# Kernel tuning notes

Hardware: AMD Instinct MI355X
Metric: run time of the kernel (lower is better)

The kernel has to match this reference:

```python
import jax, jax.numpy as jnp
import numpy as np

E = 8           # num_local_experts
H = 1024        # hidden_size
F = 1024        # moe_ffn_hidden_size (per-half; fc1 out = 2*F due to GLU)
T = 16384       # total dispatched tokens
GLU_LINEAR_OFFSET = 1.0


def setup_inputs() -> dict:
    key = jax.random.key(0)
    ks = jax.random.split(key, 7)
    s1 = 1.0 / np.sqrt(H)
    s2 = 1.0 / np.sqrt(F)
    return {
        "hidden_states": jax.random.normal(ks[0], (T, H), jnp.float32),
        "tokens_per_expert": jnp.full((E,), T // E, dtype=jnp.int64),
        "probs": jax.random.uniform(ks[1], (T,), jnp.float32),
        # expert params; torch Linear W is [out,in], stored here as [in,out] (same math)
        "W1": jax.random.uniform(ks[2], (E, H, 2 * F), jnp.float32, -s1, s1),
        "b1": jax.random.uniform(ks[3], (E, 2 * F), jnp.float32, -s1, s1),
        "W2": jax.random.uniform(ks[4], (E, F, H), jnp.float32, -s2, s2),
        "b2": jax.random.uniform(ks[5], (E, H), jnp.float32, -s2, s2),
    }


def reference(hidden_states, tokens_per_expert, probs, W1, b1, W2, b2):
    # Tokens arrive grouped contiguously by expert with equal counts (as in
    # setup_inputs), so the split/loop/cat in the torch module is exactly a
    # reshape + grouped (batched) GEMM over the expert axis.
    e = W1.shape[0]
    t, h = hidden_states.shape
    x = hidden_states.reshape(e, t // e, h)            # [E, Tpe, H]
    p = probs.reshape(e, t // e)                       # [E, Tpe]
    # fc1 (gated)
    y = jnp.einsum('eth,ehf->etf', x, W1) + b1[:, None, :]  # [E, Tpe, 2F]
    gate, lin = jnp.split(y, 2, axis=-1)
    a = jax.nn.silu(gate) * (lin + GLU_LINEAR_OFFSET)       # [E, Tpe, F]
    a = a * p[..., None]                                    # per-token scale
    # fc2
    out = jnp.einsum('etf,efh->eth', a, W2) + b2[:, None, :]
    return out.reshape(t, h)
```

## Files before the change

kernel.cpp:

```cpp
#include <hip/hip_runtime.h>
#include <hip/hip_bf16.h>
#include <stdint.h>

#define T_TOK 16384
#define H_DIM 1024
#define F_DIM 1024
#define E_NUM 8
#define TPE   2048


typedef unsigned short u16;
typedef __attribute__((ext_vector_type(8))) short bf16x8;
typedef __attribute__((ext_vector_type(4))) float f32x4;
typedef __attribute__((ext_vector_type(8))) u16 u16x8;

__device__ __forceinline__ u16 f2bf(float x) {
  unsigned int u = __float_as_uint(x);
  u = (u + 0x7fffu + ((u >> 16) & 1u)) >> 16;
  return (u16)u;
}

#define GLD16(gp, lp)                                                          \
  __builtin_amdgcn_global_load_lds(                                            \
      (const __attribute__((address_space(1))) void*)(gp),                     \
      (__attribute__((address_space(3))) void*)(lp), 16, 0, 0)

#define VMW(N) asm volatile("s_waitcnt vmcnt(" #N ")" ::: "memory");

__global__ __launch_bounds__(256) void prep_all(
    const float* __restrict__ x, const float* __restrict__ W1,
    const float* __restrict__ W2, u16* __restrict__ xbf,
    u16* __restrict__ w1t, u16* __restrict__ w2t) {
  __shared__ float tile[64][65];
  const int bid = blockIdx.x;
  const int t = threadIdx.x;

  if (bid < 4096) {
    size_t base = (size_t)bid * 4096 + (size_t)t * 16;
    const float4* s = (const float4*)(x + base);
    float4 v0 = s[0], v1 = s[1], v2 = s[2], v3 = s[3];
    u16x8 o0, o1;
    o0[0] = f2bf(v0.x); o0[1] = f2bf(v0.y); o0[2] = f2bf(v0.z); o0[3] = f2bf(v0.w);
    o0[4] = f2bf(v1.x); o0[5] = f2bf(v1.y); o0[6] = f2bf(v1.z); o0[7] = f2bf(v1.w);
    o1[0] = f2bf(v2.x); o1[1] = f2bf(v2.y); o1[2] = f2bf(v2.z); o1[3] = f2bf(v2.w);
    o1[4] = f2bf(v3.x); o1[5] = f2bf(v3.y); o1[6] = f2bf(v3.z); o1[7] = f2bf(v3.w);
    *(u16x8*)(xbf + base) = o0;
    *(u16x8*)(xbf + base + 8) = o1;
    return;
  }

  const float* src; u16* dst; int R, C, e, rt, ct;
  if (bid < 8192) {
    int id = bid - 4096;
    e = id >> 9; int r2 = id & 511; rt = r2 >> 5; ct = r2 & 31;
    src = W1; dst = w1t; R = H_DIM; C = 2 * F_DIM;
  } else {
    int id = bid - 8192;
    e = id >> 8; int r2 = id & 255; rt = r2 >> 4; ct = r2 & 15;
    src = W2; dst = w2t; R = F_DIM; C = H_DIM;
  }
  const float* s = src + (size_t)e * R * C + (size_t)(rt << 6) * C + (ct << 6);
  int lr = t >> 4, lc = (t & 15) << 2;
#pragma unroll
  for (int i = 0; i < 4; i++) {
    float4 v = *(const float4*)(s + (size_t)(lr + i * 16) * C + lc);
    tile[lr + i * 16][lc + 0] = v.x;
    tile[lr + i * 16][lc + 1] = v.y;
    tile[lr + i * 16][lc + 2] = v.z;
    tile[lr + i * 16][lc + 3] = v.w;
  }
  __syncthreads();
  u16* d = dst + (size_t)e * C * R + (size_t)(ct << 6) * R + (rt << 6);
  int orow = t >> 2, ok = (t & 3) << 4;
  u16x8 o0, o1;
#pragma unroll
  for (int i = 0; i < 8; i++) o0[i] = f2bf(tile[ok + i][orow]);
#pragma unroll
  for (int i = 0; i < 8; i++) o1[i] = f2bf(tile[ok + 8 + i][orow]);
  *(u16x8*)(d + (size_t)orow * R + ok) = o0;
  *(u16x8*)(d + (size_t)orow * R + ok + 8) = o1;
}


#define DSA2(b, h, ks)                                                         \
  _Pragma("unroll") for (int m2_ = 0; m2_ < 2; ++m2_)                          \
      aF[m2_] = *(const bf16x8*)(sm + (b) * 32768 + aRowBase +                 \
                                 ((h) * 2 + m2_) * 2048 + koff[ks]);

#define DSB4(b, ks)                                                            \
  _Pragma("unroll") for (int n_ = 0; n_ < 4; ++n_)                             \
      bF[n_] = *(const bf16x8*)(sm + 65536 + (b) * 32768 + bRowBase +          \
                                n_ * 2048 + koff[ks]);

#define MFMAP(h)                                                               \
  _Pragma("unroll") for (int n_ = 0; n_ < 4; ++n_)                             \
  _Pragma("unroll") for (int m2_ = 0; m2_ < 2; ++m2_)                          \
      acc[(h) * 2 + m2_][n_] = __builtin_amdgcn_mfma_f32_16x16x32_bf16(        \
          aF[m2_], bF[n_], acc[(h) * 2 + m2_][n_], 0, 0, 0);

#define PF_A(db, q, d) GLD16(aP[q] + (d), sm + (db) * 32768 + (q) * 16384 + tid * 16)
#define PF_B(db, q, d) GLD16(bP[q] + (d), sm + 65536 + (db) * 32768 + (q) * 16384 + tid * 16)

#define PHASEK(b, ks, h, PFC, WTC)                                             \
  do {                                                                         \
    DSA2(b, h, ks);                                                            \
    if ((h) == 0) { DSB4(b, ks); }                                             \
    PFC                                                                        \
    __builtin_amdgcn_s_setprio(1);                                             \
    MFMAP(h);                                                                  \
    __builtin_amdgcn_s_setprio(0);                                             \
    WTC                                                                        \
    __builtin_amdgcn_s_barrier();                                              \
  } while (0)

#define KLOOP_BODY                                                             \
  PF_B(0, 0, 0); PF_B(0, 1, 0);                                                \
  PF_A(0, 0, 0); PF_A(0, 1, 0);                                                \
  PF_B(1, 0, 64); PF_B(1, 1, 64);                                              \
  VMW(2)                                                                       \
  __builtin_amdgcn_s_barrier();                                                \
  for (int it = 0; it < 7; ++it) {                                             \
    PHASEK(0, 0, 0, PF_A(1, 0, 64);, );                                        \
    PHASEK(0, 0, 1, PF_A(1, 1, 64);, );                                        \
    PHASEK(0, 1, 0, , );                                                       \
    PHASEK(0, 1, 1, PF_B(0, 0, 128); PF_B(0, 1, 128);, VMW(2));                \
    PHASEK(1, 0, 0, PF_A(0, 0, 128);, );                                       \
    PHASEK(1, 0, 1, PF_A(0, 1, 128);, );                                       \
    PHASEK(1, 1, 0, , );                                                       \
    PHASEK(1, 1, 1, PF_B(1, 0, 192); PF_B(1, 1, 192);, VMW(2));                \
    _Pragma("unroll") for (int q_ = 0; q_ < 2; ++q_) {                         \
      aP[q_] += 128; bP[q_] += 128;                                            \
    }                                                                          \
  }                                                                            \
  PHASEK(0, 0, 0, PF_A(1, 0, 64);, );                                          \
  PHASEK(0, 0, 1, PF_A(1, 1, 64);, );                                          \
  PHASEK(0, 1, 0, , );                                                         \
  PHASEK(0, 1, 1, , VMW(0));                                                   \
  PHASEK(1, 0, 0, , );                                                         \
  PHASEK(1, 0, 1, , );                                                         \
  PHASEK(1, 1, 0, , );                                                         \
  PHASEK(1, 1, 1, , );

__global__ __launch_bounds__(1024) void gemm1_8p(
    const u16* __restrict__ xbf, const u16* __restrict__ w1t,
    const float* __restrict__ b1, const float* __restrict__ probs,
    u16* __restrict__ abf) {
  extern __shared__ char sm[];
  const int tid = threadIdx.x;
  const int lane = tid & 63;
  const int wid = tid >> 6;
  const int wm = wid >> 2, wn = wid & 3;
  const int bid = blockIdx.x;
  const int e = bid & 7;
  const int inner = bid >> 3;
  const int mt = inner >> 3, ct = inner & 7;
  const int tokBase = e * TPE + mt * 256;
  const int c0 = ct * 128;
  const int lrow = lane & 15, lkhi = lane >> 4;

  const u16* aP[2]; const u16* bP[2];
#pragma unroll
  for (int q = 0; q < 2; ++q) {
    int lin = q * 16384 + tid * 16;
    int lg = lin ^ (((lin >> 7) & 7) << 4);
    int row = lg >> 7, kk = (lg & 127) >> 1;
    aP[q] = xbf + (size_t)(tokBase + row) * H_DIM + kk;
    int col = (((row >> 5) & 1) << 10) + c0 + ((row >> 6) << 5) + (row & 31);
    bP[q] = w1t + (size_t)(e * 2 * F_DIM + col) * H_DIM + kk;
  }
  const int aRowBase = (wm * 64 + lrow) * 128;
  const int bRowBase = (wn * 64 + lrow) * 128;
  int koff[2];
#pragma unroll
  for (int ks = 0; ks < 2; ++ks)
    koff[ks] = ((ks << 6) | (lkhi << 4)) ^ ((lane & 7) << 4);

  f32x4 acc[4][4];
#pragma unroll
  for (int i = 0; i < 4; ++i)
#pragma unroll
    for (int j = 0; j < 4; ++j) acc[i][j] = f32x4{0.f, 0.f, 0.f, 0.f};
  bf16x8 aF[2], bF[4];

  KLOOP_BODY

#pragma unroll
  for (int j = 0; j < 2; ++j) {
    int cf = c0 + wn * 32 + j * 16 + lrow;
    float gb = b1[e * 2 * F_DIM + cf];
    float lb = b1[e * 2 * F_DIM + F_DIM + cf];
#pragma unroll
    for (int i = 0; i < 4; ++i) {
      int trow = tokBase + wm * 64 + i * 16 + lkhi * 4;
#pragma unroll
      for (int r = 0; r < 4; ++r) {
        float g = acc[i][j][r] + gb;
        float l = acc[i][j + 2][r] + lb + 1.0f;
        float p = probs[trow + r];
        float sig = 1.0f / (1.0f + __expf(-g));
        abf[(size_t)(trow + r) * F_DIM + cf] = f2bf(g * sig * l * p);
      }
    }
  }
}

__global__ __launch_bounds__(1024) void gemm2_8p(
    const u16* __restrict__ abf, const u16* __restrict__ w2t,
    const float* __restrict__ b2, float* __restrict__ out) {
  extern __shared__ char sm[];
  const int tid = threadIdx.x;
  const int lane = tid & 63;
  const int wid = tid >> 6;
  const int wm = wid >> 2, wn = wid & 3;
  const int bid = blockIdx.x;
  const int e = bid & 7;
  const int inner = bid >> 3;
  const int mt = inner >> 2, nt = inner & 3;
  const int tokBase = e * TPE + mt * 256;
  const int h0 = nt * 256;
  const int lrow = lane & 15, lkhi = lane >> 4;

  const u16* aP[2]; const u16* bP[2];
#pragma unroll
  for (int q = 0; q < 2; ++q) {
    int lin = q * 16384 + tid * 16;
    int lg = lin ^ (((lin >> 7) & 7) << 4);
    int row = lg >> 7, kk = (lg & 127) >> 1;
    aP[q] = abf + (size_t)(tokBase + row) * F_DIM + kk;
    bP[q] = w2t + (size_t)(e * H_DIM + h0 + row) * F_DIM + kk;
  }
  const int aRowBase = (wm * 64 + lrow) * 128;
  const int bRowBase = (wn * 64 + lrow) * 128;
  int koff[2];
#pragma unroll
  for (int ks = 0; ks < 2; ++ks)
    koff[ks] = ((ks << 6) | (lkhi << 4)) ^ ((lane & 7) << 4);

  f32x4 acc[4][4];
#pragma unroll
  for (int i = 0; i < 4; ++i)
#pragma unroll
    for (int j = 0; j < 4; ++j) acc[i][j] = f32x4{0.f, 0.f, 0.f, 0.f};
  bf16x8 aF[2], bF[4];

  KLOOP_BODY

#pragma unroll
  for (int j = 0; j < 4; ++j) {
    int h = h0 + wn * 64 + j * 16 + lrow;
    float bb = b2[e * H_DIM + h];
#pragma unroll
    for (int i = 0; i < 4; ++i) {
      int trow = tokBase + wm * 64 + i * 16 + lkhi * 4;
#pragma unroll
      for (int r = 0; r < 4; ++r)
        out[(size_t)(trow + r) * H_DIM + h] = acc[i][j][r] + bb;
    }
  }
}

extern "C" void kernel_launch(void* const* d_in, const int* in_sizes, int n_in,
                              void* d_out, int out_size, void* d_ws,
                              size_t ws_size, hipStream_t stream) {
  const float* x     = (const float*)d_in[0];
  const float* probs = (const float*)d_in[2];
  const float* W1    = (const float*)d_in[3];
  const float* b1    = (const float*)d_in[4];
  const float* W2    = (const float*)d_in[5];
  const float* b2    = (const float*)d_in[6];
  float* out = (float*)d_out;

  if (ws_size < 117440512u) return;
  char* ws = (char*)d_ws;
  u16* xbf = (u16*)(ws);
  u16* w1t = (u16*)(ws + 33554432);
  u16* w2t = (u16*)(ws + 67108864);
  u16* abf = (u16*)(ws + 83886080);

  (void)hipFuncSetAttribute(reinterpret_cast<const void*>(gemm1_8p),
                            hipFuncAttributeMaxDynamicSharedMemorySize, 131072);
  (void)hipFuncSetAttribute(reinterpret_cast<const void*>(gemm2_8p),
                            hipFuncAttributeMaxDynamicSharedMemorySize, 131072);

  prep_all<<<10240, 256, 0, stream>>>(x, W1, W2, xbf, w1t, w2t);
  gemm1_8p<<<E_NUM * 8 * 8, 1024, 131072, stream>>>(xbf, w1t, b1, probs, abf);
  gemm2_8p<<<E_NUM * 8 * 4, 1024, 131072, stream>>>(abf, w2t, b2, out);
}
```

Baseline: 148.7 us.

## Fuse fp32-to-bf16 activation conversion into gemm1 operand loading

Removes the separate x-to-bf16 conversion pass from the prep kernel. gemm1 now streams fp32 activations straight into LDS and converts them to bf16 while reading MFMA fragments. Its K-loop is restructured around a 64-wide K step with a matching B tile layout and pipeline. This drops a 64MB read plus 32MB write pass, but gemm1 now loads twice the A bytes per tile, does conversion ALU work in the inner loop, and runs a different LDS budget and schedule.

Result: slower. 204.3 us (+37.4%).

```diff
diff --git a/kernel.cpp b/kernel.cpp
--- a/kernel.cpp
+++ b/kernel.cpp
@@ -28,34 +28,18 @@
 #define VMW(N) asm volatile("s_waitcnt vmcnt(" #N ")" ::: "memory");
 
 __global__ __launch_bounds__(256) void prep_all(
-    const float* __restrict__ x, const float* __restrict__ W1,
-    const float* __restrict__ W2, u16* __restrict__ xbf,
+    const float* __restrict__ W1, const float* __restrict__ W2,
     u16* __restrict__ w1t, u16* __restrict__ w2t) {
   __shared__ float tile[64][65];
   const int bid = blockIdx.x;
   const int t = threadIdx.x;
 
+  const float* src; u16* dst; int R, C, e, rt, ct;
   if (bid < 4096) {
-    size_t base = (size_t)bid * 4096 + (size_t)t * 16;
-    const float4* s = (const float4*)(x + base);
-    float4 v0 = s[0], v1 = s[1], v2 = s[2], v3 = s[3];
-    u16x8 o0, o1;
-    o0[0] = f2bf(v0.x); o0[1] = f2bf(v0.y); o0[2] = f2bf(v0.z); o0[3] = f2bf(v0.w);
-    o0[4] = f2bf(v1.x); o0[5] = f2bf(v1.y); o0[6] = f2bf(v1.z); o0[7] = f2bf(v1.w);
-    o1[0] = f2bf(v2.x); o1[1] = f2bf(v2.y); o1[2] = f2bf(v2.z); o1[3] = f2bf(v2.w);
-    o1[4] = f2bf(v3.x); o1[5] = f2bf(v3.y); o1[6] = f2bf(v3.z); o1[7] = f2bf(v3.w);
-    *(u16x8*)(xbf + base) = o0;
-    *(u16x8*)(xbf + base + 8) = o1;
-    return;
-  }
-
-  const float* src; u16* dst; int R, C, e, rt, ct;
-  if (bid < 8192) {
-    int id = bid - 4096;
-    e = id >> 9; int r2 = id & 511; rt = r2 >> 5; ct = r2 & 31;
+    e = bid >> 9; int r2 = bid & 511; rt = r2 >> 5; ct = r2 & 31;
     src = W1; dst = w1t; R = H_DIM; C = 2 * F_DIM;
   } else {
-    int id = bid - 8192;
+    int id = bid - 4096;
     e = id >> 8; int r2 = id & 255; rt = r2 >> 4; ct = r2 & 15;
     src = W2; dst = w2t; R = F_DIM; C = H_DIM;
   }
@@ -81,6 +65,130 @@
   *(u16x8*)(d + (size_t)orow * R + ok + 8) = o1;
 }
 
+
+#define DSAF(b, h)                                                             \
+  _Pragma("unroll") for (int m2_ = 0; m2_ < 2; ++m2_) {                        \
+    const char* pA_ = sm + (b) * 32768 + aRowBase + ((h) * 2 + m2_) * 2048;    \
+    float4 f0_ = *(const float4*)(pA_ + koffA0);                               \
+    float4 f1_ = *(const float4*)(pA_ + koffA1);                               \
+    u16x8 w_;                                                                  \
+    w_[0] = f2bf(f0_.x); w_[1] = f2bf(f0_.y);                                  \
+    w_[2] = f2bf(f0_.z); w_[3] = f2bf(f0_.w);                                  \
+    w_[4] = f2bf(f1_.x); w_[5] = f2bf(f1_.y);                                  \
+    w_[6] = f2bf(f1_.z); w_[7] = f2bf(f1_.w);                                  \
+    aF[m2_] = (bf16x8)w_;                                                      \
+  }
+
+#define DSBF(b)                                                                \
+  _Pragma("unroll") for (int n_ = 0; n_ < 4; ++n_)                             \
+      bF[n_] = *(const bf16x8*)(sm + 65536 + (b) * 16384 + bRowBase +          \
+                                n_ * 1024 + koffB);
+
+#define MFMAF(h)                                                               \
+  _Pragma("unroll") for (int n_ = 0; n_ < 4; ++n_)                             \
+  _Pragma("unroll") for (int m2_ = 0; m2_ < 2; ++m2_)                          \
+      acc[(h) * 2 + m2_][n_] = __builtin_amdgcn_mfma_f32_16x16x32_bf16(        \
+          aF[m2_], bF[n_], acc[(h) * 2 + m2_][n_], 0, 0, 0);
+
+#define PFA_F(db, q, d)                                                        \
+  GLD16(aPf[q] + (d), sm + (db) * 32768 + (q) * 16384 + tid * 16)
+#define PFB_F(db, d) GLD16(bPf + (d), sm + 65536 + (db) * 16384 + tid * 16)
+
+#define PHF(b, h, PFC, WTC)                                                    \
+  do {                                                                         \
+    DSAF(b, h);                                                                \
+    if ((h) == 0) { DSBF(b); }                                                 \
+    PFC                                                                        \
+    __builtin_amdgcn_s_setprio(1);                                             \
+    MFMAF(h);                                                                  \
+    __builtin_amdgcn_s_setprio(0);                                             \
+    WTC                                                                        \
+    __builtin_amdgcn_s_barrier();                                              \
+  } while (0)
+
+__global__ __launch_bounds__(1024) void gemm1_8p(
+    const float* __restrict__ x, const u16* __restrict__ w1t,
+    const float* __restrict__ b1, const float* __restrict__ probs,
+    u16* __restrict__ abf) {
+  extern __shared__ char sm[];
+  const int tid = threadIdx.x;
+  const int lane = tid & 63;
+  const int wid = tid >> 6;
+  const int wm = wid >> 2, wn = wid & 3;
+  const int bid = blockIdx.x;
+  const int e = bid & 7;
+  const int inner = bid >> 3;
+  const int mt = inner >> 3, ct = inner & 7;
+  const int tokBase = e * TPE + mt * 256;
+  const int c0 = ct * 128;
+  const int lrow = lane & 15, lkhi = lane >> 4;
+
+  const float* aPf[2];
+#pragma unroll
+  for (int q = 0; q < 2; ++q) {
+    int lin = q * 16384 + tid * 16;
+    int lg = lin ^ (((lin >> 7) & 7) << 4);
+    int row = lg >> 7, kk = (lg & 127) >> 2;
+    aPf[q] = x + (size_t)(tokBase + row) * H_DIM + kk;
+  }
+  const u16* bPf;
+  {
+    int lin = tid * 16;
+    int lg = lin ^ (((lin >> 6) & 3) << 4);
+    int row = lg >> 6, kk = (lg & 63) >> 1;
+    int col = (((row >> 5) & 1) << 10) + c0 + ((row >> 6) << 5) + (row & 31);
+    bPf = w1t + (size_t)(e * 2 * F_DIM + col) * H_DIM + kk;
+  }
+  const int aRowBase = (wm * 64 + lrow) * 128;
+  const int bRowBase = (wn * 64 + lrow) * 64;
+  const int koffA0 = (lkhi * 32) ^ ((lane & 7) << 4);
+  const int koffA1 = (lkhi * 32 + 16) ^ ((lane & 7) << 4);
+  const int koffB = (lkhi * 16) ^ ((lane & 3) << 4);
+
+  f32x4 acc[4][4];
+#pragma unroll
+  for (int i = 0; i < 4; ++i)
+#pragma unroll
+    for (int j = 0; j < 4; ++j) acc[i][j] = f32x4{0.f, 0.f, 0.f, 0.f};
+  bf16x8 aF[2], bF[4];
+
+  PFB_F(0, 0);
+  PFA_F(0, 0, 0); PFA_F(0, 1, 0);
+  PFB_F(1, 32);
+  VMW(1)
+  __builtin_amdgcn_s_barrier();
+
+  for (int it = 0; it < 15; ++it) {
+    PHF(0, 0, PFA_F(1, 0, 32); PFA_F(1, 1, 32);, );
+    PHF(0, 1, PFB_F(0, 64);, VMW(1));
+    PHF(1, 0, PFA_F(0, 0, 64); PFA_F(0, 1, 64);, );
+    PHF(1, 1, PFB_F(1, 96);, VMW(1));
+    aPf[0] += 64; aPf[1] += 64; bPf += 64;
+  }
+  PHF(0, 0, PFA_F(1, 0, 32); PFA_F(1, 1, 32);, );
+  PHF(0, 1, , VMW(0));
+  PHF(1, 0, , );
+  PHF(1, 1, , );
+
+#pragma unroll
+  for (int j = 0; j < 2; ++j) {
+    int cf = c0 + wn * 32 + j * 16 + lrow;
+    float gb = b1[e * 2 * F_DIM + cf];
+    float lb = b1[e * 2 * F_DIM + F_DIM + cf];
+#pragma unroll
+    for (int i = 0; i < 4; ++i) {
+      int trow = tokBase + wm * 64 + i * 16 + lkhi * 4;
+#pragma unroll
+      for (int r = 0; r < 4; ++r) {
+        float g = acc[i][j][r] + gb;
+        float l = acc[i][j + 2][r] + lb + 1.0f;
+        float p = probs[trow + r];
+        float sig = 1.0f / (1.0f + __expf(-g));
+        abf[(size_t)(trow + r) * F_DIM + cf] = f2bf(g * sig * l * p);
+      }
+    }
+  }
+}
 
 #define DSA2(b, h, ks)                                                         \
   _Pragma("unroll") for (int m2_ = 0; m2_ < 2; ++m2_)                          \
@@ -141,69 +249,6 @@
   PHASEK(1, 1, 0, , );                                                         \
   PHASEK(1, 1, 1, , );
 
-__global__ __launch_bounds__(1024) void gemm1_8p(
-    const u16* __restrict__ xbf, const u16* __restrict__ w1t,
-    const float* __restrict__ b1, const float* __restrict__ probs,
-    u16* __restrict__ abf) {
-  extern __shared__ char sm[];
-  const int tid = threadIdx.x;
-  const int lane = tid & 63;
-  const int wid = tid >> 6;
-  const int wm = wid >> 2, wn = wid & 3;
-  const int bid = blockIdx.x;
-  const int e = bid & 7;
-  const int inner = bid >> 3;
-  const int mt = inner >> 3, ct = inner & 7;
-  const int tokBase = e * TPE + mt * 256;
-  const int c0 = ct * 128;
-  const int lrow = lane & 15, lkhi = lane >> 4;
-
-  const u16* aP[2]; const u16* bP[2];
-#pragma unroll
-  for (int q = 0; q < 2; ++q) {
-    int lin = q * 16384 + tid * 16;
-    int lg = lin ^ (((lin >> 7) & 7) << 4);
-    int row = lg >> 7, kk = (lg & 127) >> 1;
-    aP[q] = xbf + (size_t)(tokBase + row) * H_DIM + kk;
-    int col = (((row >> 5) & 1) << 10) + c0 + ((row >> 6) << 5) + (row & 31);
-    bP[q] = w1t + (size_t)(e * 2 * F_DIM + col) * H_DIM + kk;
-  }
-  const int aRowBase = (wm * 64 + lrow) * 128;
-  const int bRowBase = (wn * 64 + lrow) * 128;
-  int koff[2];
-#pragma unroll
-  for (int ks = 0; ks < 2; ++ks)
-    koff[ks] = ((ks << 6) | (lkhi << 4)) ^ ((lane & 7) << 4);
-
-  f32x4 acc[4][4];
-#pragma unroll
-  for (int i = 0; i < 4; ++i)
-#pragma unroll
-    for (int j = 0; j < 4; ++j) acc[i][j] = f32x4{0.f, 0.f, 0.f, 0.f};
-  bf16x8 aF[2], bF[4];
-
-  KLOOP_BODY
-
-#pragma unroll
-  for (int j = 0; j < 2; ++j) {
-    int cf = c0 + wn * 32 + j * 16 + lrow;
-    float gb = b1[e * 2 * F_DIM + cf];
-    float lb = b1[e * 2 * F_DIM + F_DIM + cf];
-#pragma unroll
-    for (int i = 0; i < 4; ++i) {
-      int trow = tokBase + wm * 64 + i * 16 + lkhi * 4;
-#pragma unroll
-      for (int r = 0; r < 4; ++r) {
-        float g = acc[i][j][r] + gb;
-        float l = acc[i][j + 2][r] + lb + 1.0f;
-        float p = probs[trow + r];
-        float sig = 1.0f / (1.0f + __expf(-g));
-        abf[(size_t)(trow + r) * F_DIM + cf] = f2bf(g * sig * l * p);
-      }
-    }
-  }
-}
-
 __global__ __launch_bounds__(1024) void gemm2_8p(
     const u16* __restrict__ abf, const u16* __restrict__ w2t,
     const float* __restrict__ b2, float* __restrict__ out) {
@@ -270,19 +315,18 @@
   const float* b2    = (const float*)d_in[6];
   float* out = (float*)d_out;
 
-  if (ws_size < 117440512u) return;
+  if (ws_size < 83886080u) return;
   char* ws = (char*)d_ws;
-  u16* xbf = (u16*)(ws);
-  u16* w1t = (u16*)(ws + 33554432);
-  u16* w2t = (u16*)(ws + 67108864);
-  u16* abf = (u16*)(ws + 83886080);
+  u16* w1t = (u16*)(ws);
+  u16* w2t = (u16*)(ws + 33554432);
+  u16* abf = (u16*)(ws + 50331648);
 
   (void)hipFuncSetAttribute(reinterpret_cast<const void*>(gemm1_8p),
-                            hipFuncAttributeMaxDynamicSharedMemorySize, 131072);
+                            hipFuncAttributeMaxDynamicSharedMemorySize, 98304);
   (void)hipFuncSetAttribute(reinterpret_cast<const void*>(gemm2_8p),
                             hipFuncAttributeMaxDynamicSharedMemorySize, 131072);
 
-  prep_all<<<10240, 256, 0, stream>>>(x, W1, W2, xbf, w1t, w2t);
-  gemm1_8p<<<E_NUM * 8 * 8, 1024, 131072, stream>>>(xbf, w1t, b1, probs, abf);
+  prep_all<<<6144, 256, 0, stream>>>(W1, W2, w1t, w2t);
+  gemm1_8p<<<E_NUM * 8 * 8, 1024, 98304, stream>>>(x, w1t, b1, probs, abf);
   gemm2_8p<<<E_NUM * 8 * 4, 1024, 131072, stream>>>(abf, w2t, b2, out);
 }
```
